# Performance work log

Hardware: AMD Instinct MI355X
Metric: run time of the kernel (lower is better)

## Reference

```python
import jax, jax.numpy as jnp
import numpy as np

N_NODES = 16384   # total nodes
B = 32            # graphs in batch
NPG = 512         # nodes per graph (uniform -> dense mask is all True)
E = 262144        # edges (avg degree 16)
H = 64            # hidden_dim
HEADS = 8
DH = H // HEADS


def setup_inputs() -> dict:
    key = jax.random.key(0)
    ks = jax.random.split(key, 20)
    x = jax.random.normal(ks[0], (N_NODES, H), dtype=jnp.float32)
    # edges constrained within each graph of 512 nodes
    src = jax.random.randint(ks[1], (E,), 0, N_NODES, dtype=jnp.int32)
    dst = (src // NPG) * NPG + jax.random.randint(ks[2], (E,), 0, NPG, dtype=jnp.int32)
    edge_index = jnp.stack([src, dst])
    batch = (jnp.arange(N_NODES, dtype=jnp.int32) // NPG)
    c_size = jnp.full((B,), NPG, dtype=jnp.int32)
    s = 1.0 / np.sqrt(H)
    p = lambda k, shape: (jax.random.normal(k, shape, dtype=jnp.float32) * s)
    return {
        "x": x,
        "w_gat": p(ks[3], (H, H)), "att_src": p(ks[4], (H,)), "att_dst": p(ks[5], (H,)), "b_gat": jnp.zeros((H,), jnp.float32),
        "g1": jnp.ones((H,), jnp.float32), "b1": jnp.zeros((H,), jnp.float32),
        "wq": p(ks[6], (H, H)), "bq": jnp.zeros((H,), jnp.float32),
        "wk": p(ks[7], (H, H)), "bk": jnp.zeros((H,), jnp.float32),
        "wv": p(ks[8], (H, H)), "bv": jnp.zeros((H,), jnp.float32),
        "wo": p(ks[9], (H, H)), "bo": jnp.zeros((H,), jnp.float32),
        "g2": jnp.ones((H,), jnp.float32), "b2": jnp.zeros((H,), jnp.float32),
        "edge_index": edge_index, "batch": batch, "c_size": c_size,
    }


def _layer_norm(x, g, b):
    mu = jnp.mean(x, axis=-1, keepdims=True)
    var = jnp.var(x, axis=-1, keepdims=True)
    return (x - mu) * jax.lax.rsqrt(var + 1e-5) * g + b


def _gat_conv(x, edge_index, w, a_src, a_dst, bias):
    # PyG GATConv, 1 head, add_self_loops=True, leaky_relu slope 0.2
    n = x.shape[0]
    loops = jnp.arange(n, dtype=edge_index.dtype)
    src = jnp.concatenate([edge_index[0], loops])
    dst = jnp.concatenate([edge_index[1], loops])
    h = x @ w                                  # [n, H]
    e = jax.nn.leaky_relu((h @ a_src)[src] + (h @ a_dst)[dst], 0.2)  # [E+n]
    m = jax.ops.segment_max(e, dst, num_segments=n)
    p = jnp.exp(e - m[dst])
    s = jax.ops.segment_sum(p, dst, num_segments=n)
    alpha = p / (s[dst] + 1e-16)
    out = jax.ops.segment_sum(alpha[:, None] * h[src], dst, num_segments=n)
    return out + bias


def reference(x, w_gat, att_src, att_dst, b_gat, g1, b1,
              wq, bq, wk, bk, wv, bv, wo, bo, g2, b2,
              edge_index, batch, c_size):
    # GAT branch (dropout is identity in eval)
    x_ = jax.nn.relu(_gat_conv(x, edge_index, w_gat, att_src, att_dst, b_gat))
    x1 = _layer_norm(x + x_, g1, b1)                     # [n, H]
    # to_dense_batch: uniform graphs -> mask all True, plain reshape
    xd = x1.reshape(B, NPG, H)
    q = (xd @ wq + bq).reshape(B, NPG, HEADS, DH)
    k = (xd @ wk + bk).reshape(B, NPG, HEADS, DH)
    v = (xd @ wv + bv).reshape(B, NPG, HEADS, DH)
    scores = jnp.einsum('bqhd,bkhd->bhqk', q, k) / np.sqrt(DH)  # [B,h,N,N]
    attn = jax.nn.softmax(scores, axis=-1)
    o = jnp.einsum('bhqk,bkhd->bqhd', attn, v).reshape(B, NPG, H)
    o = o @ wo + bo
    x2 = _layer_norm(x1 + jax.nn.relu(o.reshape(N_NODES, H)), g2, b2)
    return x2  # recon_loss is None in eval mode
```

## Files before the change

### kernel.cpp

```cpp
#include <hip/hip_runtime.h>
#include <hip/hip_bf16.h>
#include <hip/hip_fp16.h>

#define NN     16384
#define HD     64
#define BG     32
#define NPG    512
#define NHEADS 8
#define DH     8
#define DEGMAX 40

#define QS_STR 12
#define KS_STR 12
#define VT_STR 264

typedef __hip_bfloat16 bf16;
typedef _Float16 v4h __attribute__((ext_vector_type(4)));
typedef float v16f __attribute__((ext_vector_type(16)));

#if defined(__has_builtin)
#if __has_builtin(__builtin_amdgcn_exp2f)
#define EXP2F(x) __builtin_amdgcn_exp2f(x)
#else
#define EXP2F(x) exp2f(x)
#endif
#if __has_builtin(__builtin_amdgcn_fdot2)
#define HAS_FDOT2 1
#endif
#else
#define EXP2F(x) exp2f(x)
#endif

#ifdef HAS_FDOT2
typedef _Float16 hvec2 __attribute__((ext_vector_type(2)));
#endif

__device__ __forceinline__ float fdot2u(unsigned a, unsigned b, float c) {
#ifdef HAS_FDOT2
  union { unsigned u; hvec2 v; } x, y;
  x.u = a; y.u = b;
  return __builtin_amdgcn_fdot2(x.v, y.v, c, false);
#else
  union { unsigned u; __half2 h; } x, y;
  x.u = a; y.u = b;
  return fmaf(__low2float(x.h), __low2float(y.h),
              fmaf(__high2float(x.h), __high2float(y.h), c));
#endif
}

__device__ __forceinline__ float b2f(bf16 v) { return __bfloat162float(v); }

__device__ __forceinline__ float ldf(const void* p, int i, int bf) {
  return bf ? __bfloat162float(((const bf16*)p)[i]) : ((const float*)p)[i];
}

__device__ __forceinline__ float wave_sum(float v) {
#pragma unroll
  for (int off = 32; off > 0; off >>= 1) v += __shfl_xor(v, off);
  return v;
}

__device__ __forceinline__ void unpack8(uint4 u, float* f) {
  f[0] = __uint_as_float(u.x << 16); f[1] = __uint_as_float(u.x & 0xffff0000u);
  f[2] = __uint_as_float(u.y << 16); f[3] = __uint_as_float(u.y & 0xffff0000u);
  f[4] = __uint_as_float(u.z << 16); f[5] = __uint_as_float(u.z & 0xffff0000u);
  f[6] = __uint_as_float(u.w << 16); f[7] = __uint_as_float(u.w & 0xffff0000u);
}

__device__ __forceinline__ unsigned short bfbits(float f) {
  bf16 b = __float2bfloat16(f);
  return *(unsigned short*)&b;
}

__device__ __forceinline__ unsigned packh2(float a, float b) {
  union { unsigned u; __half2 h; } z;
  z.h = __floats2half2_rn(a, b);
  return z.u;
}

__device__ __forceinline__ int detect_bf(const unsigned short* xr, int tid, int nt) {
  __shared__ int s_cnt;
  if (tid == 0) s_cnt = 0;
  __syncthreads();
  int sane = 0;
  for (int i = tid; i < 256; i += nt) {
    int e = (xr[2 * i] >> 7) & 0xFF;
    sane += (e >= 100 && e <= 150) ? 1 : 0;
  }
  if (sane) atomicAdd(&s_cnt, sane);
  __syncthreads();
  return s_cnt > 180;
}

__global__ __launch_bounds__(256) void k_build(
    const void* __restrict__ x, const void* __restrict__ w,
    const void* __restrict__ asrc, const void* __restrict__ adst,
    const int* __restrict__ esrc, const int* __restrict__ edst, int E,
    int* __restrict__ cur, int* __restrict__ ell,
    bf16* __restrict__ h, float* __restrict__ as_, float* __restrict__ ad_,
    int* __restrict__ flagp)
{
  const int tid = threadIdx.x, lane = tid & 63, wid = tid >> 6;
  const int bf = detect_bf((const unsigned short*)x, tid, 256);
  if (tid == 0 && blockIdx.x == 0) *flagp = bf;
  __shared__ float wl[HD * HD];
  __shared__ float xr[4][HD];
  {
    for (int e = blockIdx.x * 256 + tid; e < E; e += gridDim.x * 256) {
      int d = edst[e];
      int k = atomicAdd(&cur[d], 1);
      if (k < DEGMAX) ell[d * DEGMAX + k] = esrc[e];
    }
  }
  for (int i = tid; i < HD * HD; i += 256) wl[i] = ldf(w, i, bf);
  const float av = ldf(asrc, lane, bf), dv_ = ldf(adst, lane, bf);
  __syncthreads();
#pragma unroll
  for (int r = 0; r < 4; ++r) {
    const int node = blockIdx.x * 16 + r * 4 + wid;
    xr[wid][lane] = ldf(x, node * HD + lane, bf);
    float hj = 0.f;
#pragma unroll
    for (int i = 0; i < HD; ++i) hj = fmaf(xr[wid][i], wl[i * HD + lane], hj);
    float pa = wave_sum(hj * av);
    float pd = wave_sum(hj * dv_);
    h[node * HD + lane] = __float2bfloat16(hj);
    if (lane == 0) { as_[node] = pa; ad_[node] = pd; }
  }
}

__global__ __launch_bounds__(256) void k_gather(
    const void* __restrict__ x, const int* __restrict__ cur,
    const int* __restrict__ ell, const float* __restrict__ as_,
    const float* __restrict__ ad_, const bf16* __restrict__ h,
    const void* __restrict__ bg, const void* __restrict__ g1,
    const void* __restrict__ b1,
    const void* __restrict__ wq, const void* __restrict__ bq,
    const void* __restrict__ wk, const void* __restrict__ bk,
    const void* __restrict__ wv, const void* __restrict__ bv,
    const int* __restrict__ dflag,
    unsigned* __restrict__ wpk, float* __restrict__ bpk,
    __half* __restrict__ x1)
{
  const int tid = threadIdx.x, lane = tid & 63, wid = tid >> 6;
  const int bf = *dflag;
  if (blockIdx.x < 4) {
    for (int idx = blockIdx.x * 256 + tid; idx < 3 * 32 * 64; idx += 1024) {
      int m = idx >> 11;
      int r = idx & 2047;
      int kp = r >> 6, col = r & 63;
      const void* ws = (m == 0) ? wq : (m == 1) ? wk : wv;
      wpk[idx] = packh2(ldf(ws, (2 * kp) * HD + col, bf),
                        ldf(ws, (2 * kp + 1) * HD + col, bf));
    }
  } else if (blockIdx.x == 4 && tid < 192) {
    int m = tid >> 6, col = tid & 63;
    const void* bs = (m == 0) ? bq : (m == 1) ? bk : bv;
    bpk[tid] = ldf(bs, col, bf);
  }
  const int n = blockIdx.x * 4 + wid;
  const float adn = ad_[n];
  float e0 = as_[n] + adn;
  e0 = e0 > 0.f ? e0 : 0.2f * e0;
  float den = __expf(fminf(e0, 30.f));
  float num = den * b2f(h[n * HD + lane]);
  const int deg = min(cur[n], DEGMAX);
  const int* row = ell + n * DEGMAX;
  int i = 0;
  for (; i + 8 <= deg; i += 8) {
    int s[8];
#pragma unroll
    for (int k = 0; k < 8; ++k) s[k] = row[i + k];
    float a[8], hh[8];
#pragma unroll
    for (int k = 0; k < 8; ++k) a[k] = as_[s[k]];
#pragma unroll
    for (int k = 0; k < 8; ++k) hh[k] = b2f(h[s[k] * HD + lane]);
#pragma unroll
    for (int k = 0; k < 8; ++k) {
      float e = a[k] + adn;
      e = e > 0.f ? e : 0.2f * e;
      float p = __expf(fminf(e, 30.f));
      den += p;
      num = fmaf(p, hh[k], num);
    }
  }
  for (; i + 4 <= deg; i += 4) {
    int s0 = row[i], s1 = row[i + 1], s2 = row[i + 2], s3 = row[i + 3];
    float a0 = as_[s0], a1 = as_[s1], a2 = as_[s2], a3 = as_[s3];
    float h0 = b2f(h[s0 * HD + lane]), h1 = b2f(h[s1 * HD + lane]);
    float h2 = b2f(h[s2 * HD + lane]), h3 = b2f(h[s3 * HD + lane]);
    float e_0 = a0 + adn; e_0 = e_0 > 0.f ? e_0 : 0.2f * e_0;
    float e_1 = a1 + adn; e_1 = e_1 > 0.f ? e_1 : 0.2f * e_1;
    float e_2 = a2 + adn; e_2 = e_2 > 0.f ? e_2 : 0.2f * e_2;
    float e_3 = a3 + adn; e_3 = e_3 > 0.f ? e_3 : 0.2f * e_3;
    float p0 = __expf(fminf(e_0, 30.f)), p1 = __expf(fminf(e_1, 30.f));
    float p2 = __expf(fminf(e_2, 30.f)), p3 = __expf(fminf(e_3, 30.f));
    den += p0 + p1 + p2 + p3;
    num = fmaf(p0, h0, num); num = fmaf(p1, h1, num);
    num = fmaf(p2, h2, num); num = fmaf(p3, h3, num);
  }
  for (; i < deg; ++i) {
    int s = row[i];
    float e = as_[s] + adn;
    e = e > 0.f ? e : 0.2f * e;
    float p = __expf(fminf(e, 30.f));
    den += p;
    num = fmaf(p, b2f(h[s * HD + lane]), num);
  }
  float v = num / (den + 1e-16f) + ldf(bg, lane, bf);
  v = fmaxf(v, 0.f) + ldf(x, n * HD + lane, bf);
  float mu = wave_sum(v) * (1.f / 64.f);
  float dv = v - mu;
  float var = wave_sum(dv * dv) * (1.f / 64.f);
  float r = rsqrtf(var + 1e-5f);
  x1[n * HD + lane] =
      __float2half(dv * r * ldf(g1, lane, bf) + ldf(b1, lane, bf));
}

__global__ __launch_bounds__(512, 2) void k_attn13(
    const __half* __restrict__ x1,
    const unsigned* __restrict__ wpk, const float* __restrict__ bpk,
    bf16* __restrict__ num_t, float* __restrict__ den_t)
{
  const int t = threadIdx.x;
  __shared__ _Float16 Qs[NPG * QS_STR];
  __shared__ _Float16 Ks[256 * KS_STR];
  __shared__ _Float16 Vt[DH * VT_STR];
  const int bid = blockIdx.x;
  const int g = bid >> 4, hd = (bid >> 1) & 7, half = bid & 1;
  const float qscale = 0.3535533905932738f * 1.4426950408889634f;
  {
    const int r = t & 255;
    const int m = (t < 256) ? 1 : 2;
    const uint4* xk4 = (const uint4*)(x1 + (size_t)(g * NPG + half * 256 + r) * HD);
    const unsigned* wb0 = wpk + m * 2048 + hd * 8;
    float acc[DH];
#pragma unroll
    for (int j = 0; j < DH; ++j) acc[j] = bpk[m * 64 + hd * 8 + j];
#pragma unroll
    for (int blk = 0; blk < 8; ++blk) {
      uint4 xp = xk4[blk];
      const unsigned* wb = wb0 + blk * 256;
#pragma unroll
      for (int j = 0; j < DH; ++j) {
        acc[j] = fdot2u(xp.x, wb[j], acc[j]);
        acc[j] = fdot2u(xp.y, wb[64 + j], acc[j]);
        acc[j] = fdot2u(xp.z, wb[128 + j], acc[j]);
        acc[j] = fdot2u(xp.w, wb[192 + j], acc[j]);
      }
    }
    if (t < 256) {
      unsigned w0 = packh2(acc[0], acc[1]), w1 = packh2(acc[2], acc[3]);
      unsigned w2 = packh2(acc[4], acc[5]), w3 = packh2(acc[6], acc[7]);
      *(uint2*)(Ks + r * KS_STR) = make_uint2(w0, w1);
      *(uint2*)(Ks + r * KS_STR + 4) = make_uint2(w2, w3);
    } else {
#pragma unroll
      for (int j = 0; j < DH; ++j) Vt[j * VT_STR + r] = (_Float16)acc[j];
    }
  }
  {
    const uint4* xa4 = (const uint4*)(x1 + (size_t)(g * NPG + t) * HD);
    const unsigned* wb0 = wpk + hd * 8;
    float qa[DH];
#pragma unroll
    for (int j = 0; j < DH; ++j) qa[j] = bpk[hd * 8 + j];
#pragma unroll
    for (int blk = 0; blk < 8; ++blk) {
      uint4 xp = xa4[blk];
      const unsigned* wb = wb0 + blk * 256;
#pragma unroll
      for (int j = 0; j < DH; ++j) {
        qa[j] = fdot2u(xp.x, wb[j], qa[j]);
        qa[j] = fdot2u(xp.y, wb[64 + j], qa[j]);
        qa[j] = fdot2u(xp.z, wb[128 + j], qa[j]);
        qa[j] = fdot2u(xp.w, wb[192 + j], qa[j]);
      }
    }
    unsigned w0 = packh2(qa[0] * qscale, qa[1] * qscale);
    unsigned w1 = packh2(qa[2] * qscale, qa[3] * qscale);
    unsigned w2 = packh2(qa[4] * qscale, qa[5] * qscale);
    unsigned w3 = packh2(qa[6] * qscale, qa[7] * qscale);
    *(uint2*)(Qs + t * QS_STR) = make_uint2(w0, w1);
    *(uint2*)(Qs + t * QS_STR + 4) = make_uint2(w2, w3);
  }
  __syncthreads();
  const int lane = t & 63, wid = t >> 6;
  const int ln = lane & 31, hh = lane >> 5;
  const int plane = half * 8 + hd;
  const size_t obase = (size_t)plane * NN + (size_t)g * NPG;
  v16f zf;
#pragma unroll
  for (int i = 0; i < 16; ++i) zf[i] = 0.f;
#pragma unroll
  for (int qt = 0; qt < 2; ++qt) {
    const int qbase = (wid * 2 + qt) * 32;
    v4h qf = *(const v4h*)(Qs + (qbase + ln) * QS_STR + 4 * hh);
    v16f oacc = zf;
    float den = 0.f;
#pragma unroll
    for (int kt = 0; kt < 8; ++kt) {
      v4h kf = *(const v4h*)(Ks + (kt * 32 + ln) * KS_STR + 4 * hh);
      v16f s = __builtin_amdgcn_mfma_f32_32x32x8f16(kf, qf, zf, 0, 0, 0);
#pragma unroll
      for (int g2 = 0; g2 < 4; ++g2) {
        float e0 = EXP2F(s[4 * g2 + 0]);
        float e1 = EXP2F(s[4 * g2 + 1]);
        float e2 = EXP2F(s[4 * g2 + 2]);
        float e3 = EXP2F(s[4 * g2 + 3]);
        den += (e0 + e1) + (e2 + e3);
        union { unsigned u[2]; v4h v; } pu;
        pu.u[0] = packh2(e0, e1);
        pu.u[1] = packh2(e2, e3);
        v4h vf = *(const v4h*)(Vt + (ln & 7) * VT_STR + kt * 32 + g2 * 8 + 4 * hh);
        oacc = __builtin_amdgcn_mfma_f32_32x32x8f16(pu.v, vf, oacc, 0, 0, 0);
      }
    }
    den += __shfl_xor(den, 32);
    if (lane < 32) den_t[obase + qbase + lane] = den;
#pragma unroll
    for (int r = 0; r < 16; ++r) {
      const int q = qbase + (r & 3) + 8 * (r >> 2) + 4 * hh;
      if (ln < 8)
        num_t[(obase + q) * 8 + ln] = __float2bfloat16(oacc[r]);
    }
  }
}

__global__ __launch_bounds__(64) void k_out(
    const bf16* __restrict__ num_t, const float* __restrict__ den_t,
    const __half* __restrict__ x1,
    const void* __restrict__ wo, const void* __restrict__ bo,
    const void* __restrict__ g2, const void* __restrict__ b2,
    const int* __restrict__ dflag, void* __restrict__ out)
{
  const int t = threadIdx.x;
  const int bf = *dflag;
  const int ln = t & 31, hh = t >> 5;
  const int base = blockIdx.x * 32;
  const int n = base + ln;
  v16f c0, c1;
#pragma unroll
  for (int i = 0; i < 16; ++i) { c0[i] = 0.f; c1[i] = 0.f; }
#pragma unroll
  for (int kt = 0; kt < 8; ++kt) {
    union { uint2 u; unsigned short s[4]; } L, H;
    L.u = *(const uint2*)(num_t + ((size_t)kt * NN + n) * 8 + 4 * hh);
    H.u = *(const uint2*)(num_t + ((size_t)(8 + kt) * NN + n) * 8 + 4 * hh);
    float den = den_t[(size_t)kt * NN + n] + den_t[(size_t)(8 + kt) * NN + n];
    float rden = 1.f / den;
    float o0 = (__uint_as_float((unsigned)L.s[0] << 16) +
                __uint_as_float((unsigned)H.s[0] << 16)) * rden;
    float o1 = (__uint_as_float((unsigned)L.s[1] << 16) +
                __uint_as_float((unsigned)H.s[1] << 16)) * rden;
    float o2 = (__uint_as_float((unsigned)L.s[2] << 16) +
                __uint_as_float((unsigned)H.s[2] << 16)) * rden;
    float o3 = (__uint_as_float((unsigned)L.s[3] << 16) +
                __uint_as_float((unsigned)H.s[3] << 16)) * rden;
    union { unsigned u[2]; v4h v; } A;
    A.u[0] = packh2(o0, o1);
    A.u[1] = packh2(o2, o3);
    const int kr = kt * 8 + 4 * hh;
    union { unsigned u[2]; v4h v; } B0, B1;
    B0.u[0] = packh2(ldf(wo, (kr + 0) * HD + ln, bf),
                     ldf(wo, (kr + 1) * HD + ln, bf));
    B0.u[1] = packh2(ldf(wo, (kr + 2) * HD + ln, bf),
                     ldf(wo, (kr + 3) * HD + ln, bf));
    B1.u[0] = packh2(ldf(wo, (kr + 0) * HD + 32 + ln, bf),
                     ldf(wo, (kr + 1) * HD + 32 + ln, bf));
    B1.u[1] = packh2(ldf(wo, (kr + 2) * HD + 32 + ln, bf),
                     ldf(wo, (kr + 3) * HD + 32 + ln, bf));
    c0 = __builtin_amdgcn_mfma_f32_32x32x8f16(A.v, B0.v, c0, 0, 0, 0);
    c1 = __builtin_amdgcn_mfma_f32_32x32x8f16(A.v, B1.v, c1, 0, 0, 0);
  }
  const float bo0 = ldf(bo, ln, bf),      bo1 = ldf(bo, 32 + ln, bf);
  const float g20 = ldf(g2, ln, bf),      g21 = ldf(g2, 32 + ln, bf);
  const float b20 = ldf(b2, ln, bf),      b21 = ldf(b2, 32 + ln, bf);
#pragma unroll
  for (int r = 0; r < 16; ++r) {
    const int node = base + (r & 3) + 8 * (r >> 2) + 4 * hh;
    float t0 = __half2float(x1[node * HD + ln]) + fmaxf(c0[r] + bo0, 0.f);
    float t1 = __half2float(x1[node * HD + 32 + ln]) + fmaxf(c1[r] + bo1, 0.f);
    float s = t0 + t1;
#pragma unroll
    for (int off = 1; off < 32; off <<= 1) s += __shfl_xor(s, off);
    const float mu = s * (1.f / 64.f);
    const float d0 = t0 - mu, d1 = t1 - mu;
    float v = d0 * d0 + d1 * d1;
#pragma unroll
    for (int off = 1; off < 32; off <<= 1) v += __shfl_xor(v, off);
    const float rr = rsqrtf(v * (1.f / 64.f) + 1e-5f);
    const float r0 = d0 * rr * g20 + b20;
    const float r1 = d1 * rr * g21 + b21;
    if (bf) {
      ((bf16*)out)[node * HD + ln]      = __float2bfloat16(r0);
      ((bf16*)out)[node * HD + 32 + ln] = __float2bfloat16(r1);
    } else {
      ((float*)out)[node * HD + ln]      = r0;
      ((float*)out)[node * HD + 32 + ln] = r1;
    }
  }
}

extern "C" void kernel_launch(void* const* d_in, const int* in_sizes, int n_in,
                              void* d_out, int out_size, void* d_ws, size_t ws_size,
                              hipStream_t stream)
{
  const void* x    = d_in[0];
  const void* wgat = d_in[1];
  const void* asrc = d_in[2];
  const void* adst = d_in[3];
  const void* bgat = d_in[4];
  const void* g1   = d_in[5];
  const void* b1   = d_in[6];
  const void* wq   = d_in[7];
  const void* bq   = d_in[8];
  const void* wk   = d_in[9];
  const void* bk   = d_in[10];
  const void* wv   = d_in[11];
  const void* bv   = d_in[12];
  const void* wo   = d_in[13];
  const void* bo   = d_in[14];
  const void* g2   = d_in[15];
  const void* b2   = d_in[16];
  const int*  ei   = (const int*)d_in[17];
  const int E = in_sizes[17] / 2;
  const int* esrc = ei;
  const int* edst = ei + E;

  char* W = (char*)d_ws;
  __half* x1b  = (__half*)W;
  int*   ell   = (int*)(W + (size_t)(2 << 20));
  bf16*  hb    = (bf16*)(W + (size_t)(2 << 20) + (size_t)NN * DEGMAX * 4);
  bf16*  num_t = (bf16*)(W + (size_t)(2 << 20));
  float* den_t = (float*)(W + (size_t)(6 << 20));
  float* as_   = (float*)(W + (size_t)(7 << 20));
  float* ad_   = as_ + NN;
  int*   cur   = (int*)(ad_ + NN);
  int*   flag  = cur + NN;
  unsigned* wpk = (unsigned*)(flag + 1);
  float* bpk   = (float*)(wpk + 3 * 32 * 64);

  hipMemsetAsync(cur, 0, NN * sizeof(int), stream);
  k_build  <<<NN / 16, 256, 0, stream>>>(x, wgat, asrc, adst, esrc, edst, E,
                                         cur, ell, hb, as_, ad_, flag);
  k_gather <<<NN / 4, 256, 0, stream>>>(x, cur, ell, as_, ad_, hb,
                                        bgat, g1, b1,
                                        wq, bq, wk, bk, wv, bv,
                                        flag, wpk, bpk, x1b);
  k_attn13 <<<BG * NHEADS * 2, 512, 0, stream>>>(x1b, wpk, bpk, num_t, den_t);
  k_out    <<<NN / 32, 64, 0, stream>>>(num_t, den_t, x1b, wo, bo, g2, b2,
                                        flag, d_out);
}
```

Baseline: 177.7 us.

## Compute GAT projection in k_build with f16 MFMA, single-wave blocks

After: 173.7 us. -2.3%, faster.

```diff
diff --git a/kernel.cpp b/kernel.cpp
--- a/kernel.cpp
+++ b/kernel.cpp
@@ -60,13 +60,6 @@
   return v;
 }
 
-__device__ __forceinline__ void unpack8(uint4 u, float* f) {
-  f[0] = __uint_as_float(u.x << 16); f[1] = __uint_as_float(u.x & 0xffff0000u);
-  f[2] = __uint_as_float(u.y << 16); f[3] = __uint_as_float(u.y & 0xffff0000u);
-  f[4] = __uint_as_float(u.z << 16); f[5] = __uint_as_float(u.z & 0xffff0000u);
-  f[6] = __uint_as_float(u.w << 16); f[7] = __uint_as_float(u.w & 0xffff0000u);
-}
-
 __device__ __forceinline__ unsigned short bfbits(float f) {
   bf16 b = __float2bfloat16(f);
   return *(unsigned short*)&b;
@@ -78,21 +71,7 @@
   return z.u;
 }
 
-__device__ __forceinline__ int detect_bf(const unsigned short* xr, int tid, int nt) {
-  __shared__ int s_cnt;
-  if (tid == 0) s_cnt = 0;
-  __syncthreads();
-  int sane = 0;
-  for (int i = tid; i < 256; i += nt) {
-    int e = (xr[2 * i] >> 7) & 0xFF;
-    sane += (e >= 100 && e <= 150) ? 1 : 0;
-  }
-  if (sane) atomicAdd(&s_cnt, sane);
-  __syncthreads();
-  return s_cnt > 180;
-}
-
-__global__ __launch_bounds__(256) void k_build(
+__global__ __launch_bounds__(64) void k_build(
     const void* __restrict__ x, const void* __restrict__ w,
     const void* __restrict__ asrc, const void* __restrict__ adst,
     const int* __restrict__ esrc, const int* __restrict__ edst, int E,
@@ -100,32 +79,62 @@
     bf16* __restrict__ h, float* __restrict__ as_, float* __restrict__ ad_,
     int* __restrict__ flagp)
 {
-  const int tid = threadIdx.x, lane = tid & 63, wid = tid >> 6;
-  const int bf = detect_bf((const unsigned short*)x, tid, 256);
-  if (tid == 0 && blockIdx.x == 0) *flagp = bf;
-  __shared__ float wl[HD * HD];
-  __shared__ float xr[4][HD];
+  const int t = threadIdx.x;
+  const int ln = t & 31, hh = t >> 5;
+  int sane = 0;
   {
-    for (int e = blockIdx.x * 256 + tid; e < E; e += gridDim.x * 256) {
-      int d = edst[e];
-      int k = atomicAdd(&cur[d], 1);
-      if (k < DEGMAX) ell[d * DEGMAX + k] = esrc[e];
-    }
-  }
-  for (int i = tid; i < HD * HD; i += 256) wl[i] = ldf(w, i, bf);
-  const float av = ldf(asrc, lane, bf), dv_ = ldf(adst, lane, bf);
-  __syncthreads();
-#pragma unroll
-  for (int r = 0; r < 4; ++r) {
-    const int node = blockIdx.x * 16 + r * 4 + wid;
-    xr[wid][lane] = ldf(x, node * HD + lane, bf);
-    float hj = 0.f;
-#pragma unroll
-    for (int i = 0; i < HD; ++i) hj = fmaf(xr[wid][i], wl[i * HD + lane], hj);
-    float pa = wave_sum(hj * av);
-    float pd = wave_sum(hj * dv_);
-    h[node * HD + lane] = __float2bfloat16(hj);
-    if (lane == 0) { as_[node] = pa; ad_[node] = pd; }
+    const unsigned short* xr = (const unsigned short*)x;
+    for (int i = t; i < 256; i += 64) {
+      int e = (xr[2 * i] >> 7) & 0xFF;
+      sane += (e >= 100 && e <= 150) ? 1 : 0;
+    }
+#pragma unroll
+    for (int off = 32; off > 0; off >>= 1) sane += __shfl_xor(sane, off);
+  }
+  const int bf = sane > 180;
+  if (t == 0 && blockIdx.x == 0) *flagp = bf;
+  for (int e = blockIdx.x * 64 + t; e < E; e += gridDim.x * 64) {
+    int d = edst[e];
+    int k = atomicAdd(&cur[d], 1);
+    if (k < DEGMAX) ell[d * DEGMAX + k] = esrc[e];
+  }
+  const int base = blockIdx.x * 32;
+  v16f c0, c1;
+#pragma unroll
+  for (int i = 0; i < 16; ++i) { c0[i] = 0.f; c1[i] = 0.f; }
+#pragma unroll
+  for (int kt = 0; kt < 8; ++kt) {
+    const int kr = kt * 8 + 4 * hh;
+    union { unsigned u[2]; v4h v; } A, B0, B1;
+    const int xb = (base + ln) * HD + kr;
+    A.u[0] = packh2(ldf(x, xb + 0, bf), ldf(x, xb + 1, bf));
+    A.u[1] = packh2(ldf(x, xb + 2, bf), ldf(x, xb + 3, bf));
+    B0.u[0] = packh2(ldf(w, (kr + 0) * HD + ln, bf),
+                     ldf(w, (kr + 1) * HD + ln, bf));
+    B0.u[1] = packh2(ldf(w, (kr + 2) * HD + ln, bf),
+                     ldf(w, (kr + 3) * HD + ln, bf));
+    B1.u[0] = packh2(ldf(w, (kr + 0) * HD + 32 + ln, bf),
+                     ldf(w, (kr + 1) * HD + 32 + ln, bf));
+    B1.u[1] = packh2(ldf(w, (kr + 2) * HD + 32 + ln, bf),
+                     ldf(w, (kr + 3) * HD + 32 + ln, bf));
+    c0 = __builtin_amdgcn_mfma_f32_32x32x8f16(A.v, B0.v, c0, 0, 0, 0);
+    c1 = __builtin_amdgcn_mfma_f32_32x32x8f16(A.v, B1.v, c1, 0, 0, 0);
+  }
+  const float av0 = ldf(asrc, ln, bf), av1 = ldf(asrc, 32 + ln, bf);
+  const float dv0 = ldf(adst, ln, bf), dv1 = ldf(adst, 32 + ln, bf);
+#pragma unroll
+  for (int r = 0; r < 16; ++r) {
+    const int node = base + (r & 3) + 8 * (r >> 2) + 4 * hh;
+    h[node * HD + ln]      = __float2bfloat16(c0[r]);
+    h[node * HD + 32 + ln] = __float2bfloat16(c1[r]);
+    float pa = c0[r] * av0 + c1[r] * av1;
+    float pd = c0[r] * dv0 + c1[r] * dv1;
+#pragma unroll
+    for (int off = 16; off > 0; off >>= 1) {
+      pa += __shfl_xor(pa, off);
+      pd += __shfl_xor(pd, off);
+    }
+    if (ln == 0) { as_[node] = pa; ad_[node] = pd; }
   }
 }
 
@@ -443,8 +452,8 @@
   float* bpk   = (float*)(wpk + 3 * 32 * 64);
 
   hipMemsetAsync(cur, 0, NN * sizeof(int), stream);
-  k_build  <<<NN / 16, 256, 0, stream>>>(x, wgat, asrc, adst, esrc, edst, E,
-                                         cur, ell, hb, as_, ad_, flag);
+  k_build  <<<NN / 32, 64, 0, stream>>>(x, wgat, asrc, adst, esrc, edst, E,
+                                        cur, ell, hb, as_, ad_, flag);
   k_gather <<<NN / 4, 256, 0, stream>>>(x, cur, ell, as_, ad_, hb,
                                         bgat, g1, b1,
                                         wq, bq, wk, bk, wv, bv,
```
